# Kernel tuning notes

Measured on AMD Instinct MI355X. Metric: run time of the kernel, lower is better.

## Reference

```python
import jax, jax.numpy as jnp
import numpy as np

MAX_DISP = 4
STRIDE = 2

def setup_inputs() -> dict:
    key = jax.random.key(0)
    k1, k2 = jax.random.split(key)
    B, C, H, W = 8, 256, 96, 192
    in1 = jax.random.normal(k1, (B, C, H, W), dtype=jnp.float32)
    in2 = jax.random.normal(k2, (B, C, H, W), dtype=jnp.float32)
    return {"in1": in1, "in2": in2}

def reference(in1, in2):
    # Correlation (cost volume) layer: for each displacement (dy, dx) on a
    # stride-2 grid in [-max_disp, max_disp], compute channel-mean of
    # in1 * shifted(in2). Output: [B, D^2, H, W] with D = max_disp/stride*2 + 1.
    B, C, H, W = in1.shape
    md, st = MAX_DISP, STRIDE
    in2p = jnp.pad(in2, ((0, 0), (0, 0), (md, md), (md, md)))  # zero pad H, W
    offsets = range(0, 2 * md + 1, st)  # {0,2,4,6,8} -> 5 per axis
    # dy outer, dx inner matches torch.meshgrid('ij') flatten order.
    corr = [jnp.mean(in1 * in2p[:, :, dy:dy + H, dx:dx + W], axis=1)
            for dy in offsets for dx in offsets]
    return jnp.stack(corr, axis=1)  # [B, 25, H, W]
```

## Files before the change

### kernel.cpp

```cpp
#include <hip/hip_runtime.h>

#define BB 8
#define CH 256
#define HH 96
#define WW 192
#define HW (HH*WW)
#define ND 25
#define NTHR 320
#define UNR 4

__global__ __launch_bounds__(NTHR, 4)
void corr_kernel(const float* __restrict__ in1, const float* __restrict__ in2,
                 float* __restrict__ out) {
  const int bid = blockIdx.x;
  const int swz = (bid & 7) * 72 + (bid >> 3);
  const int b   = swz / 72;
  const int rem = swz - b * 72;
  const int h0  = (rem / 3) * 4;
  const int w0  = (rem % 3) * 64;

  const int t    = threadIdx.x;
  const int g    = t >> 6;
  const int lane = t & 63;
  const int r    = lane >> 4;
  const int i    = lane & 15;
  const int h    = h0 + r;
  const int wq   = w0 + (i << 2);
  const int y    = h + 2 * g - 4;

  const bool rowok = ((unsigned)y < HH);
  const bool lok   = rowok && (wq >= 4);
  const bool rok   = rowok && (wq <= WW - 8);
  const int  yc    = y < 0 ? 0 : (y > HH - 1 ? HH - 1 : y);

  const size_t bpl = (size_t)b * CH * HW;
  const float* p1 = in1 + bpl + (size_t)h * WW + wq;
  const float* pm = in2 + bpl + (size_t)yc * WW + wq;
  const float* pl = pm - (lok ? 4 : 0);
  const float* pr = pm + (rok ? 4 : 0);

  const float4 z4 = make_float4(0.f, 0.f, 0.f, 0.f);
  float4 acc[5];
  #pragma unroll
  for (int j = 0; j < 5; ++j) acc[j] = z4;

  for (int base = 0; base < CH; base += UNR) {
    float4 A[UNR], WL[UNR], WM[UNR], WR[UNR];
    #pragma unroll
    for (int u = 0; u < UNR; ++u) {
      const size_t adv = (size_t)u * HW;
      A[u]  = *(const float4*)(p1 + adv);
      WL[u] = *(const float4*)(pl + adv);
      WM[u] = *(const float4*)(pm + adv);
      WR[u] = *(const float4*)(pr + adv);
    }
    #pragma unroll
    for (int u = 0; u < UNR; ++u) {
      float wv[12];
      wv[0]  = lok   ? WL[u].x : 0.f;
      wv[1]  = lok   ? WL[u].y : 0.f;
      wv[2]  = lok   ? WL[u].z : 0.f;
      wv[3]  = lok   ? WL[u].w : 0.f;
      wv[4]  = rowok ? WM[u].x : 0.f;
      wv[5]  = rowok ? WM[u].y : 0.f;
      wv[6]  = rowok ? WM[u].z : 0.f;
      wv[7]  = rowok ? WM[u].w : 0.f;
      wv[8]  = rok   ? WR[u].x : 0.f;
      wv[9]  = rok   ? WR[u].y : 0.f;
      wv[10] = rok   ? WR[u].z : 0.f;
      wv[11] = rok   ? WR[u].w : 0.f;
      const float4 a = A[u];
      #pragma unroll
      for (int j = 0; j < 5; ++j) {
        float4& Ac = acc[j];
        Ac.x = fmaf(a.x, wv[0 + 2*j], Ac.x);
        Ac.y = fmaf(a.y, wv[1 + 2*j], Ac.y);
        Ac.z = fmaf(a.z, wv[2 + 2*j], Ac.z);
        Ac.w = fmaf(a.w, wv[3 + 2*j], Ac.w);
      }
    }
    p1 += (size_t)UNR * HW;
    pl += (size_t)UNR * HW;
    pm += (size_t)UNR * HW;
    pr += (size_t)UNR * HW;
  }

  const float scale = 1.0f / CH;
  float* pout = out + ((size_t)(b * ND + g * 5) * HH + h) * WW + wq;
  #pragma unroll
  for (int j = 0; j < 5; ++j) {
    float4 v;
    v.x = acc[j].x * scale; v.y = acc[j].y * scale;
    v.z = acc[j].z * scale; v.w = acc[j].w * scale;
    *(float4*)(pout + (size_t)j * HW) = v;
  }
}

extern "C" void kernel_launch(void* const* d_in, const int* in_sizes, int n_in,
                              void* d_out, int out_size, void* d_ws, size_t ws_size,
                              hipStream_t stream) {
  const float* in1 = (const float*)d_in[0];
  const float* in2 = (const float*)d_in[1];
  float* out = (float*)d_out;
  corr_kernel<<<dim3(BB * 72), NTHR, 0, stream>>>(in1, in2, out);
}
```

Baseline: 188.7 us.

## Split channel reduction across grid y with workspace partials and reduce kernel

The channel loop is split into G chunks along a second grid dimension. Each chunk writes partial sums to a workspace buffer, and a separate kernel sums the partials into the output. Out-of-range loads now point at a zeroed buffer with zero stride instead of being masked with selects, and a sched_barrier separates the load and FMA phases. The goal is more blocks in flight than the original 576, which is few for this GPU. The cost is extra write and read traffic for the partial buffers (G full-size outputs), plus an extra memset and a second launch.

```diff
diff --git a/kernel.cpp b/kernel.cpp
--- a/kernel.cpp
+++ b/kernel.cpp
@@ -8,10 +8,12 @@
 #define ND 25
 #define NTHR 320
 #define UNR 4
+#define OUTSZ (BB*ND*HH*WW)
 
 __global__ __launch_bounds__(NTHR, 4)
-void corr_kernel(const float* __restrict__ in1, const float* __restrict__ in2,
-                 float* __restrict__ out) {
+void corr_partial(const float* __restrict__ in1, const float* __restrict__ in2,
+                  const float* __restrict__ zp, float* __restrict__ part,
+                  int cCount) {
   const int bid = blockIdx.x;
   const int swz = (bid & 7) * 72 + (bid >> 3);
   const int b   = swz / 72;
@@ -20,55 +22,49 @@
   const int w0  = (rem % 3) * 64;
 
   const int t    = threadIdx.x;
-  const int g    = t >> 6;
+  const int dg   = t >> 6;
   const int lane = t & 63;
   const int r    = lane >> 4;
   const int i    = lane & 15;
   const int h    = h0 + r;
   const int wq   = w0 + (i << 2);
-  const int y    = h + 2 * g - 4;
+  const int y    = h + 2 * dg - 4;
 
   const bool rowok = ((unsigned)y < HH);
   const bool lok   = rowok && (wq >= 4);
   const bool rok   = rowok && (wq <= WW - 8);
-  const int  yc    = y < 0 ? 0 : (y > HH - 1 ? HH - 1 : y);
 
-  const size_t bpl = (size_t)b * CH * HW;
+  const int cBegin = blockIdx.y * cCount;
+  const size_t bpl = (size_t)b * CH * HW + (size_t)cBegin * HW;
+
   const float* p1 = in1 + bpl + (size_t)h * WW + wq;
-  const float* pm = in2 + bpl + (size_t)yc * WW + wq;
-  const float* pl = pm - (lok ? 4 : 0);
-  const float* pr = pm + (rok ? 4 : 0);
+  const float* pm = rowok ? in2 + bpl + (size_t)y * WW + wq : zp;
+  const float* pl = lok ? pm - 4 : zp;
+  const float* pr = rok ? pm + 4 : zp;
+  const size_t sm = rowok ? (size_t)HW : 0;
+  const size_t sl = lok   ? (size_t)HW : 0;
+  const size_t sr = rok   ? (size_t)HW : 0;
 
-  const float4 z4 = make_float4(0.f, 0.f, 0.f, 0.f);
   float4 acc[5];
   #pragma unroll
-  for (int j = 0; j < 5; ++j) acc[j] = z4;
+  for (int j = 0; j < 5; ++j) acc[j] = make_float4(0.f, 0.f, 0.f, 0.f);
 
-  for (int base = 0; base < CH; base += UNR) {
+  #pragma unroll 1
+  for (int base = 0; base < cCount; base += UNR) {
     float4 A[UNR], WL[UNR], WM[UNR], WR[UNR];
     #pragma unroll
     for (int u = 0; u < UNR; ++u) {
-      const size_t adv = (size_t)u * HW;
-      A[u]  = *(const float4*)(p1 + adv);
-      WL[u] = *(const float4*)(pl + adv);
-      WM[u] = *(const float4*)(pm + adv);
-      WR[u] = *(const float4*)(pr + adv);
+      A[u]  = *(const float4*)(p1 + (size_t)u * HW);
+      WL[u] = *(const float4*)(pl + (size_t)u * sl);
+      WM[u] = *(const float4*)(pm + (size_t)u * sm);
+      WR[u] = *(const float4*)(pr + (size_t)u * sr);
     }
+    __builtin_amdgcn_sched_barrier(0);
     #pragma unroll
     for (int u = 0; u < UNR; ++u) {
-      float wv[12];
-      wv[0]  = lok   ? WL[u].x : 0.f;
-      wv[1]  = lok   ? WL[u].y : 0.f;
-      wv[2]  = lok   ? WL[u].z : 0.f;
-      wv[3]  = lok   ? WL[u].w : 0.f;
-      wv[4]  = rowok ? WM[u].x : 0.f;
-      wv[5]  = rowok ? WM[u].y : 0.f;
-      wv[6]  = rowok ? WM[u].z : 0.f;
-      wv[7]  = rowok ? WM[u].w : 0.f;
-      wv[8]  = rok   ? WR[u].x : 0.f;
-      wv[9]  = rok   ? WR[u].y : 0.f;
-      wv[10] = rok   ? WR[u].z : 0.f;
-      wv[11] = rok   ? WR[u].w : 0.f;
+      const float wv[12] = { WL[u].x, WL[u].y, WL[u].z, WL[u].w,
+                             WM[u].x, WM[u].y, WM[u].z, WM[u].w,
+                             WR[u].x, WR[u].y, WR[u].z, WR[u].w };
       const float4 a = A[u];
       #pragma unroll
       for (int j = 0; j < 5; ++j) {
@@ -80,13 +76,14 @@
       }
     }
     p1 += (size_t)UNR * HW;
-    pl += (size_t)UNR * HW;
-    pm += (size_t)UNR * HW;
-    pr += (size_t)UNR * HW;
+    pl += (size_t)UNR * sl;
+    pm += (size_t)UNR * sm;
+    pr += (size_t)UNR * sr;
   }
 
   const float scale = 1.0f / CH;
-  float* pout = out + ((size_t)(b * ND + g * 5) * HH + h) * WW + wq;
+  float* pout = part + (size_t)blockIdx.y * OUTSZ
+              + ((size_t)(b * ND + dg * 5) * HH + h) * WW + wq;
   #pragma unroll
   for (int j = 0; j < 5; ++j) {
     float4 v;
@@ -96,11 +93,37 @@
   }
 }
 
+__global__ void corr_reduce(const float* __restrict__ part,
+                            float* __restrict__ out, int G) {
+  const int n4 = OUTSZ / 4;
+  int i = blockIdx.x * 256 + threadIdx.x;
+  if (i >= n4) return;
+  const float4* p = (const float4*)part;
+  float4 s = p[i];
+  for (int g = 1; g < G; ++g) {
+    float4 v = p[(size_t)g * n4 + i];
+    s.x += v.x; s.y += v.y; s.z += v.z; s.w += v.w;
+  }
+  ((float4*)out)[i] = s;
+}
+
 extern "C" void kernel_launch(void* const* d_in, const int* in_sizes, int n_in,
                               void* d_out, int out_size, void* d_ws, size_t ws_size,
                               hipStream_t stream) {
   const float* in1 = (const float*)d_in[0];
   const float* in2 = (const float*)d_in[1];
   float* out = (float*)d_out;
-  corr_kernel<<<dim3(BB * 72), NTHR, 0, stream>>>(in1, in2, out);
+
+  int G = 4;
+  while (G > 1 && ws_size < (size_t)G * OUTSZ * sizeof(float) + 256) G >>= 1;
+  float* part = (G == 1) ? out : (float*)d_ws;
+  float* zp = (float*)((char*)d_ws +
+                       ((G == 1) ? 0 : (size_t)G * OUTSZ * sizeof(float)));
+  hipMemsetAsync(zp, 0, 256, stream);
+
+  dim3 grid(BB * 72, G);
+  corr_partial<<<grid, NTHR, 0, stream>>>(in1, in2, zp, part, CH / G);
+  if (G > 1) {
+    corr_reduce<<<(OUTSZ/4 + 255)/256, 256, 0, stream>>>((const float*)d_ws, out, G);
+  }
 }
```

Result: faster. 173.0 us (-8.3%).
